# Kernel tuning notes

Measured on AMD Instinct MI355X. Metric: run time of the kernel, lower is better.

Reference implementation:

```python
import jax, jax.numpy as jnp
import numpy as np

EPS = 1e-5


def setup_inputs() -> dict:
    key = jax.random.key(0)
    k1, k2, k3 = jax.random.split(key, 3)
    B, C, H, W = 32, 64, 32, 32
    N = 16  # out_planes: number of independent BatchNorm2d branches
    x = jax.random.normal(k1, (B, C, H, W), dtype=jnp.float32)
    # per-branch affine params (torch init is gamma=1, beta=0; randomize for testing)
    gamma = jax.random.uniform(k2, (N, C), dtype=jnp.float32, minval=0.5, maxval=1.5)
    beta = jax.random.normal(k3, (N, C), dtype=jnp.float32) * 0.1
    return {"x": x, "gamma": gamma, "beta": beta}


def reference(x, gamma, beta):
    # All N BatchNorm2d branches see the identical input, so the batch
    # mean/var reduction over (B, H, W) is computed ONCE and shared.
    mean = jnp.mean(x, axis=(0, 2, 3))                    # [C]
    var = jnp.mean((x - mean[None, :, None, None]) ** 2,  # biased var, as torch BN
                   axis=(0, 2, 3))                        # [C]
    inv = jax.lax.rsqrt(var + EPS)                        # [C]
    xhat = (x - mean[None, :, None, None]) * inv[None, :, None, None]  # [B,C,H,W]
    # Per-branch affine, then concat along channel dim -> [B, N*C, H, W]
    out = gamma[None, :, :, None, None] * xhat[:, None] + beta[None, :, :, None, None]
    B, N, C, H, W = out.shape
    return out.reshape(B, N * C, H, W)
```

## Files before the change

### kernel.cpp

```cpp
#include <hip/hip_runtime.h>

#define CH      64
#define BATCH   32
#define NBR     16
#define HW      1024
#define NPC     32768

__global__ void __launch_bounds__(256) bn_partial(const float* __restrict__ x,
                                                  float* __restrict__ partials) {
    const int c = blockIdx.x & 63;
    const int g = blockIdx.x >> 6;
    const int t = threadIdx.x;

    float s = 0.f, sq = 0.f;
#pragma unroll
    for (int bb = 0; bb < 4; ++bb) {
        const int batch = g * 4 + bb;
        const float4 v = ((const float4*)x)[(batch * CH + c) * 256 + t];
        s  += v.x + v.y + v.z + v.w;
        sq += v.x * v.x + v.y * v.y + v.z * v.z + v.w * v.w;
    }

#pragma unroll
    for (int off = 32; off > 0; off >>= 1) {
        s  += __shfl_down(s, off);
        sq += __shfl_down(sq, off);
    }
    __shared__ float ls[4], lq[4];
    const int wave = t >> 6, lane = t & 63;
    if (lane == 0) { ls[wave] = s; lq[wave] = sq; }
    __syncthreads();
    if (t == 0) {
        const float S = ls[0] + ls[1] + ls[2] + ls[3];
        const float Q = lq[0] + lq[1] + lq[2] + lq[3];
        partials[(g * CH + c) * 2 + 0] = S;
        partials[(g * CH + c) * 2 + 1] = Q;
    }
}

__global__ void __launch_bounds__(1024) bn_finalize(const float* __restrict__ partials,
                                                    const float* __restrict__ gamma,
                                                    const float* __restrict__ beta,
                                                    float* __restrict__ scale,
                                                    float* __restrict__ shift) {
    const int t = threadIdx.x;
    const int c = t & 63;
    float S = 0.f, Q = 0.f;
#pragma unroll
    for (int g = 0; g < 8; ++g) {
        S += partials[(g * CH + c) * 2 + 0];
        Q += partials[(g * CH + c) * 2 + 1];
    }
    const float mean = S * (1.0f / NPC);
    const float var  = Q * (1.0f / NPC) - mean * mean;
    const float inv  = rsqrtf(var + 1e-5f);
    const float a    = gamma[t] * inv;
    scale[t] = a;
    shift[t] = beta[t] - a * mean;
}

__global__ void __launch_bounds__(256) bn_apply(const float* __restrict__ x,
                                                const float* __restrict__ scale,
                                                const float* __restrict__ shift,
                                                float* __restrict__ out) {
    const int idx = blockIdx.x * 256 + threadIdx.x;
    const int b   = idx >> 14;
    const int c   = (idx >> 8) & 63;
    const int hw4 = idx & 255;

    const float4 v = ((const float4*)x)[idx];
    float4* o4 = (float4*)out;

#pragma unroll
    for (int n = 0; n < NBR; ++n) {
        const float a = scale[n * CH + c];
        const float s = shift[n * CH + c];
        float4 o;
        o.x = a * v.x + s;
        o.y = a * v.y + s;
        o.z = a * v.z + s;
        o.w = a * v.w + s;
        o4[((b * 1024 + n * CH + c) << 8) + hw4] = o;
    }
}

extern "C" void kernel_launch(void* const* d_in, const int* in_sizes, int n_in,
                              void* d_out, int out_size, void* d_ws, size_t ws_size,
                              hipStream_t stream) {
    const float* x     = (const float*)d_in[0];
    const float* gamma = (const float*)d_in[1];
    const float* beta  = (const float*)d_in[2];
    float* out = (float*)d_out;
    float* ws  = (float*)d_ws;

    float* partials = ws;
    float* scale    = ws + 1024;
    float* shift    = ws + 2048;

    bn_partial <<<512, 256, 0, stream>>>(x, partials);
    bn_finalize<<<1, 1024, 0, stream>>>(partials, gamma, beta, scale, shift);
    bn_apply   <<<2048, 256, 0, stream>>>(x, scale, shift, out);
}
```

Measured before the change: 146.1 us.

## Fold BN finalize into apply kernel and restructure apply to stream contiguous outputs

Drops the single-block finalize kernel and launches two kernels instead of three. Each apply block recomputes mean, variance and its per-branch scale/shift for 32 channels from the per-(batch,channel) partials and holds them in shared memory. Apply blocks now own one (batch, branch, channel-half) and loop over 32 channels, writing one contiguous 128KB output region per block, where before each thread scattered 16 strided stores. The partial kernel now emits one wave-level sum per (batch, channel), removing its shared-memory reduction. The cost is redundant finalize work in every apply block and x being re-read once per branch, which relies on cache hits.

```diff
diff --git a/kernel.cpp b/kernel.cpp
--- a/kernel.cpp
+++ b/kernel.cpp
@@ -3,84 +3,77 @@
 #define CH      64
 #define BATCH   32
 #define NBR     16
-#define HW      1024
-#define NPC     32768
+#define HW4     256
 
 __global__ void __launch_bounds__(256) bn_partial(const float* __restrict__ x,
                                                   float* __restrict__ partials) {
-    const int c = blockIdx.x & 63;
-    const int g = blockIdx.x >> 6;
-    const int t = threadIdx.x;
+    const int b    = blockIdx.x & 31;
+    const int cg   = blockIdx.x >> 5;
+    const int wave = threadIdx.x >> 6;
+    const int lane = threadIdx.x & 63;
+    const int c    = cg * 4 + wave;
 
+    const float4* xp = (const float4*)x + (b * CH + c) * HW4;
     float s = 0.f, sq = 0.f;
 #pragma unroll
-    for (int bb = 0; bb < 4; ++bb) {
-        const int batch = g * 4 + bb;
-        const float4 v = ((const float4*)x)[(batch * CH + c) * 256 + t];
+    for (int i = 0; i < 4; ++i) {
+        const float4 v = xp[i * 64 + lane];
         s  += v.x + v.y + v.z + v.w;
         sq += v.x * v.x + v.y * v.y + v.z * v.z + v.w * v.w;
     }
-
 #pragma unroll
     for (int off = 32; off > 0; off >>= 1) {
         s  += __shfl_down(s, off);
         sq += __shfl_down(sq, off);
     }
-    __shared__ float ls[4], lq[4];
-    const int wave = t >> 6, lane = t & 63;
-    if (lane == 0) { ls[wave] = s; lq[wave] = sq; }
-    __syncthreads();
-    if (t == 0) {
-        const float S = ls[0] + ls[1] + ls[2] + ls[3];
-        const float Q = lq[0] + lq[1] + lq[2] + lq[3];
-        partials[(g * CH + c) * 2 + 0] = S;
-        partials[(g * CH + c) * 2 + 1] = Q;
+    if (lane == 0) {
+        partials[(b * CH + c) * 2 + 0] = s;
+        partials[(b * CH + c) * 2 + 1] = sq;
     }
 }
 
-__global__ void __launch_bounds__(1024) bn_finalize(const float* __restrict__ partials,
-                                                    const float* __restrict__ gamma,
-                                                    const float* __restrict__ beta,
-                                                    float* __restrict__ scale,
-                                                    float* __restrict__ shift) {
-    const int t = threadIdx.x;
-    const int c = t & 63;
-    float S = 0.f, Q = 0.f;
+__global__ void __launch_bounds__(256) bn_apply(const float* __restrict__ x,
+                                                const float* __restrict__ partials,
+                                                const float* __restrict__ gamma,
+                                                const float* __restrict__ beta,
+                                                float* __restrict__ out) {
+    const int bid  = blockIdx.x;
+    const int b    = bid & 31;
+    const int n    = (bid >> 5) & 15;
+    const int half = bid >> 9;
+    const int t    = threadIdx.x;
+
+    __shared__ float sa[32], ss[32];
+    if (t < 32) {
+        const int c = half * 32 + t;
+        float S = 0.f, Q = 0.f;
 #pragma unroll
-    for (int g = 0; g < 8; ++g) {
-        S += partials[(g * CH + c) * 2 + 0];
-        Q += partials[(g * CH + c) * 2 + 1];
+        for (int bb = 0; bb < 32; ++bb) {
+            S += partials[(bb * CH + c) * 2 + 0];
+            Q += partials[(bb * CH + c) * 2 + 1];
+        }
+        const float mean = S * (1.0f / 32768.0f);
+        const float var  = Q * (1.0f / 32768.0f) - mean * mean;
+        const float inv  = rsqrtf(var + 1e-5f);
+        const float a    = gamma[n * CH + c] * inv;
+        sa[t] = a;
+        ss[t] = beta[n * CH + c] - a * mean;
     }
-    const float mean = S * (1.0f / NPC);
-    const float var  = Q * (1.0f / NPC) - mean * mean;
-    const float inv  = rsqrtf(var + 1e-5f);
-    const float a    = gamma[t] * inv;
-    scale[t] = a;
-    shift[t] = beta[t] - a * mean;
-}
+    __syncthreads();
 
-__global__ void __launch_bounds__(256) bn_apply(const float* __restrict__ x,
-                                                const float* __restrict__ scale,
-                                                const float* __restrict__ shift,
-                                                float* __restrict__ out) {
-    const int idx = blockIdx.x * 256 + threadIdx.x;
-    const int b   = idx >> 14;
-    const int c   = (idx >> 8) & 63;
-    const int hw4 = idx & 255;
-
-    const float4 v = ((const float4*)x)[idx];
-    float4* o4 = (float4*)out;
-
-#pragma unroll
-    for (int n = 0; n < NBR; ++n) {
-        const float a = scale[n * CH + c];
-        const float s = shift[n * CH + c];
+    const float4* xp = (const float4*)x   + (b * CH + half * 32) * HW4 + t;
+    float4*       op = (float4*)out + ((b * NBR + n) * CH + half * 32) * HW4 + t;
+#pragma unroll 4
+    for (int cc = 0; cc < 32; ++cc) {
+        const float a = sa[cc];
+        const float s = ss[cc];
+        const float4 v = xp[cc * HW4];
         float4 o;
-        o.x = a * v.x + s;
-        o.y = a * v.y + s;
-        o.z = a * v.z + s;
-        o.w = a * v.w + s;
-        o4[((b * 1024 + n * CH + c) << 8) + hw4] = o;
+        o.x = fmaf(a, v.x, s);
+        o.y = fmaf(a, v.y, s);
+        o.z = fmaf(a, v.z, s);
+        o.w = fmaf(a, v.w, s);
+        op[cc * HW4] = o;
     }
 }
 
@@ -94,10 +87,7 @@
     float* ws  = (float*)d_ws;
 
     float* partials = ws;
-    float* scale    = ws + 1024;
-    float* shift    = ws + 2048;
 
-    bn_partial <<<512, 256, 0, stream>>>(x, partials);
-    bn_finalize<<<1, 1024, 0, stream>>>(partials, gamma, beta, scale, shift);
-    bn_apply   <<<2048, 256, 0, stream>>>(x, scale, shift, out);
+    bn_partial<<<512, 256, 0, stream>>>(x, partials);
+    bn_apply  <<<1024, 256, 0, stream>>>(x, partials, gamma, beta, out);
 }
```

Result: no change. 145.9 us (-0.1%).
